# Kernel tuning notes

Hardware: AMD Instinct MI355X
Metric: run time of the kernel (lower is better)

Reference implementation:

```python
import jax, jax.numpy as jnp
import numpy as np

N_HEADS = 16
ROPE_BASE = 10000.0

def rotate_half(x):
    x1, x2 = jnp.split(x, 2, axis=-1)
    return jnp.concatenate([-x2, x1], axis=-1)

def rope_cos_sin(seq_len, head_dim, dtype):
    inv_freq = 1.0 / (ROPE_BASE ** (jnp.arange(0, head_dim, 2, dtype=jnp.float32) / head_dim))
    t = jnp.arange(seq_len, dtype=jnp.float32)
    freqs = jnp.einsum('i,j->ij', t, inv_freq)           # [S, hd/2]
    emb = jnp.concatenate([freqs, freqs], axis=-1)        # [S, hd]
    return jnp.cos(emb).astype(dtype), jnp.sin(emb).astype(dtype)

def setup_inputs() -> dict:
    key = jax.random.key(0)
    ks = jax.random.split(key, 5)
    B, S, D = 2, 2048, 2048
    x = jax.random.normal(ks[0], (B, S, D), dtype=jnp.float32)
    Wq = jax.random.normal(ks[1], (D, D), dtype=jnp.float32) * (D ** -0.5)
    Wk = jax.random.normal(ks[2], (D, D), dtype=jnp.float32) * (D ** -0.5)
    Wv = jax.random.normal(ks[3], (D, D), dtype=jnp.float32) * (D ** -0.5)
    Wo = jax.random.normal(ks[4], (D, D), dtype=jnp.float32) * (D ** -0.5)
    return {'x': x, 'Wq': Wq, 'Wk': Wk, 'Wv': Wv, 'Wo': Wo}

def reference(x, Wq, Wk, Wv, Wo):
    B, S, D = x.shape
    H = N_HEADS
    hd = D // H
    scale = hd ** -0.5
    # projections (torch Linear: x @ W.T), split heads -> [B, H, S, hd]
    def proj(W):
        return (x @ W.T).reshape(B, S, H, hd).transpose(0, 2, 1, 3)
    q, k, v = proj(Wq), proj(Wk), proj(Wv)
    # RoPE
    cos, sin = rope_cos_sin(S, hd, x.dtype)               # [S, hd]
    cos = cos[None, None, :, :]
    sin = sin[None, None, :, :]
    q = q * cos + rotate_half(q) * sin
    k = k * cos + rotate_half(k) * sin
    # scores + causal mask + fp32 softmax
    scores = jnp.einsum('bhqd,bhkd->bhqk', q, k) * scale
    causal = jnp.triu(jnp.ones((S, S), dtype=bool), k=1)  # True above diag
    scores = jnp.where(causal[None, None, :, :], -jnp.inf, scores)
    attn = jax.nn.softmax(scores.astype(jnp.float32), axis=-1).astype(q.dtype)
    out = jnp.einsum('bhqk,bhkd->bhqd', attn, v)
    out = out.transpose(0, 2, 1, 3).reshape(B, S, D)
    return out @ Wo.T
```

## Files before the change

### kernel.cpp

```cpp
#include <hip/hip_runtime.h>
#include <hip/hip_bf16.h>
#include <math.h>

#define BB 2
#define SS 2048
#define DD 2048
#define HH 16
#define HD 128
#define MM (BB * SS)
#define SCALE 0.08838834764831845f

typedef __attribute__((ext_vector_type(8))) __bf16 bf16x8;
typedef __attribute__((ext_vector_type(4))) float f32x4;
typedef __attribute__((ext_vector_type(8))) unsigned short ushort8v;

__device__ __forceinline__ float bf2f(unsigned short u) {
    union { unsigned int u; float f; } x;
    x.u = ((unsigned int)u) << 16;
    return x.f;
}
__device__ __forceinline__ unsigned short f2bf(float f) {
    union { float f; unsigned int u; } x;
    x.f = f;
    unsigned int r = x.u + 0x7FFFu + ((x.u >> 16) & 1u);
    return (unsigned short)(r >> 16);
}

__global__ __launch_bounds__(256) void cast_all(const float* __restrict__ x,
                                                const float* __restrict__ Wq,
                                                const float* __restrict__ Wk,
                                                const float* __restrict__ Wv,
                                                const float* __restrict__ Wo,
                                                unsigned short* __restrict__ xb,
                                                unsigned short* __restrict__ wqb) {
    int bid = blockIdx.x;
    const float* src;
    unsigned short* dst;
    int idx;
    if (bid < 8192) {
        src = x; dst = xb;
        idx = bid * 256 + threadIdx.x;
    } else {
        int seg = (bid - 8192) >> 12;
        idx = ((bid - 8192) & 4095) * 256 + threadIdx.x;
        src = (seg == 0) ? Wq : (seg == 1) ? Wk : (seg == 2) ? Wv : Wo;
        dst = wqb + (size_t)seg * ((size_t)DD * DD);
    }
    float4 v = ((const float4*)src)[idx];
    ushort4 o;
    o.x = f2bf(v.x); o.y = f2bf(v.y); o.z = f2bf(v.z); o.w = f2bf(v.w);
    ((ushort4*)dst)[idx] = o;
}

__global__ __launch_bounds__(64) void rope_table_kernel(float* __restrict__ cost,
                                                        float* __restrict__ sint) {
    int s = blockIdx.x;
    int i = threadIdx.x;
    float inv = powf(10000.0f, -((float)(2 * i) / 128.0f));
    float ang = (float)s * inv;
    cost[s * 64 + i] = cosf(ang);
    sint[s * 64 + i] = sinf(ang);
}

#define GEMM_BODY(A_, W_, m0_, n0_, K_, ACC_)                                      \
    for (int k0 = 0; k0 < (K_); k0 += 32) {                                        \
        __syncthreads();                                                           \
        _Pragma("unroll")                                                          \
        for (int i = 0; i < 2; ++i) {                                              \
            int c = 2 * w + i;                                                     \
            int row = c * 16 + (l >> 2);                                           \
            const unsigned short* ga = (A_) + (size_t)((m0_) + row) * (K_) + k0 + (l & 3) * 8; \
            __builtin_amdgcn_global_load_lds(                                      \
                (const __attribute__((address_space(1))) unsigned int*)ga,         \
                (__attribute__((address_space(3))) unsigned int*)(As + c * 512),   \
                16, 0, 0);                                                         \
            const unsigned short* gb = (W_) + (size_t)((n0_) + row) * (K_) + k0 + (l & 3) * 8; \
            __builtin_amdgcn_global_load_lds(                                      \
                (const __attribute__((address_space(1))) unsigned int*)gb,         \
                (__attribute__((address_space(3))) unsigned int*)(Bs + c * 512),   \
                16, 0, 0);                                                         \
        }                                                                          \
        __syncthreads();                                                           \
        bf16x8 af[4], bfr[4];                                                      \
        _Pragma("unroll")                                                          \
        for (int i = 0; i < 4; ++i) {                                              \
            af[i]  = *(const bf16x8*)&As[(wr + i * 16 + rlane) * 32 + g * 8];      \
            bfr[i] = *(const bf16x8*)&Bs[(wc + i * 16 + rlane) * 32 + g * 8];      \
        }                                                                          \
        _Pragma("unroll")                                                          \
        for (int i = 0; i < 4; ++i)                                                \
            _Pragma("unroll")                                                      \
            for (int j = 0; j < 4; ++j)                                            \
                ACC_[i][j] = __builtin_amdgcn_mfma_f32_16x16x32_bf16(af[i], bfr[j], ACC_[i][j], 0, 0, 0); \
    }

__global__ __launch_bounds__(256) void gemm_qkv(const unsigned short* __restrict__ A,
                                                const unsigned short* __restrict__ Wc,
                                                unsigned short* __restrict__ qkv) {
    __shared__ unsigned short As[128 * 32];
    __shared__ unsigned short Bs[128 * 32];
    int t = threadIdx.x, w = t >> 6, l = t & 63;
    int rlane = l & 15, g = l >> 4;
    int flat = (int)blockIdx.y * 48 + (int)blockIdx.x;
    int swz = (flat & 7) * 192 + (flat >> 3);
    int n0 = (swz % 48) * 128;
    int m0 = (swz / 48) * 128;
    int wr = (w >> 1) * 64, wc = (w & 1) * 64;
    f32x4 acc[4][4] = {};
    GEMM_BODY(A, Wc, m0, n0, 2048, acc)
    unsigned short* base = qkv + (size_t)(n0 >> 11) * ((size_t)MM * DD);
    int nc0 = n0 & 2047;
#pragma unroll
    for (int i = 0; i < 4; ++i)
#pragma unroll
        for (int r = 0; r < 4; ++r) {
            int row = m0 + wr + i * 16 + g * 4 + r;
#pragma unroll
            for (int j = 0; j < 4; ++j) {
                int col = nc0 + wc + j * 16 + rlane;
                base[(size_t)row * DD + col] = f2bf(acc[i][j][r]);
            }
        }
}

__global__ __launch_bounds__(256) void gemm_out(const unsigned short* __restrict__ A,
                                                const unsigned short* __restrict__ W,
                                                float* __restrict__ C) {
    __shared__ unsigned short As[128 * 32];
    __shared__ unsigned short Bs[128 * 32];
    int t = threadIdx.x, w = t >> 6, l = t & 63;
    int rlane = l & 15, g = l >> 4;
    int flat = (int)blockIdx.y * 16 + (int)blockIdx.x;
    int swz = (flat & 7) * 64 + (flat >> 3);
    int n0 = (swz % 16) * 128;
    int m0 = (swz / 16) * 128;
    int wr = (w >> 1) * 64, wc = (w & 1) * 64;
    f32x4 acc[4][4] = {};
    GEMM_BODY(A, W, m0, n0, 2048, acc)
#pragma unroll
    for (int i = 0; i < 4; ++i)
#pragma unroll
        for (int r = 0; r < 4; ++r) {
            int row = m0 + wr + i * 16 + g * 4 + r;
#pragma unroll
            for (int j = 0; j < 4; ++j) {
                int col = n0 + wc + j * 16 + rlane;
                C[(size_t)row * DD + col] = acc[i][j][r];
            }
        }
}

__global__ __launch_bounds__(256) void rope_apply_kernel(unsigned short* __restrict__ arr,
                                                         const float* __restrict__ cost,
                                                         const float* __restrict__ sint) {
    int idx = blockIdx.x * 256 + threadIdx.x;
    int i4 = (idx & 15) * 4;
    int h = (idx >> 4) & 15;
    int row = idx >> 8;
    int s = row & (SS - 1);
    float4 c  = *(const float4*)&cost[s * 64 + i4];
    float4 sn = *(const float4*)&sint[s * 64 + i4];
    size_t p0 = (size_t)row * DD + h * HD + i4;
    ushort4 lo = *(ushort4*)&arr[p0];
    ushort4 hi = *(ushort4*)&arr[p0 + 64];
    ushort4 olo, ohi;
    olo.x = f2bf(bf2f(lo.x) * c.x - bf2f(hi.x) * sn.x);
    olo.y = f2bf(bf2f(lo.y) * c.y - bf2f(hi.y) * sn.y);
    olo.z = f2bf(bf2f(lo.z) * c.z - bf2f(hi.z) * sn.z);
    olo.w = f2bf(bf2f(lo.w) * c.w - bf2f(hi.w) * sn.w);
    ohi.x = f2bf(bf2f(hi.x) * c.x + bf2f(lo.x) * sn.x);
    ohi.y = f2bf(bf2f(hi.y) * c.y + bf2f(lo.y) * sn.y);
    ohi.z = f2bf(bf2f(hi.z) * c.z + bf2f(lo.z) * sn.z);
    ohi.w = f2bf(bf2f(hi.w) * c.w + bf2f(lo.w) * sn.w);
    *(ushort4*)&arr[p0] = olo;
    *(ushort4*)&arr[p0 + 64] = ohi;
}

__global__ __launch_bounds__(256, 3) void mfma_attn(const unsigned short* __restrict__ qm,
                                                    const unsigned short* __restrict__ km,
                                                    const unsigned short* __restrict__ vm,
                                                    unsigned short* __restrict__ om) {
    __shared__ unsigned short Ks[2][64 * 128];
    __shared__ unsigned short Vt[128 * 64];
    __shared__ unsigned short Ps[4][16 * 40];

    int t = threadIdx.x;
    int w = t >> 6;
    int l = t & 63;
    int l15 = l & 15;
    int g = l >> 4;

    int pj = blockIdx.x;
    int h = blockIdx.y;
    int b = blockIdx.z;
    size_t bbase = (size_t)b * SS * DD + (size_t)h * HD;

    int vk0 = 2 * (t >> 3);
    int vd8 = t & 7;
    int cbase = (l15 >> 2) & 3;
    int gsw = (g ^ (l15 & 3)) * 8;

    auto stage_k = [&](int kt2, int buf) {
#pragma unroll
        for (int s = 0; s < 4; ++s) {
            int row = w * 16 + s * 4 + (l >> 4);
            int c = ((l >> 2) & 3) ^ s;
            int gg = (l & 3) ^ (l >> 4);
            const unsigned short* ga = km + bbase +
                (size_t)(kt2 * 64 + row) * DD + c * 32 + gg * 8;
            __builtin_amdgcn_global_load_lds(
                (const __attribute__((address_space(1))) unsigned int*)ga,
                (__attribute__((address_space(3))) unsigned int*)(&Ks[buf][(w * 16 + s * 4) * 128]),
                16, 0, 0);
        }
    };

    ushort8v va[2], vb[2];
    auto load_v = [&](int kt2) {
        const unsigned short* vsrc = vm + bbase + (size_t)(kt2 * 64 + vk0) * DD + vd8 * 8;
        va[0] = *(const ushort8v*)(vsrc);
        vb[0] = *(const ushort8v*)(vsrc + DD);
        va[1] = *(const ushort8v*)(vsrc + 64);
        vb[1] = *(const ushort8v*)(vsrc + DD + 64);
    };
    auto write_v = [&]() {
#pragma unroll
        for (int i = 0; i < 2; ++i)
#pragma unroll
            for (int j = 0; j < 8; ++j) {
                int d = (vd8 + 8 * i) * 8 + j;
                int swz = (vk0 >> 3) ^ ((d >> 3) & 7);
                unsigned int pack = (unsigned int)va[i][j] | ((unsigned int)vb[i][j] << 16);
                *(unsigned int*)&Vt[d * 64 + swz * 8 + (vk0 & 7)] = pack;
            }
    };

#pragma unroll 1
    for (int half = 0; half < 2; ++half) {
        int qt = half ? pj : (31 - pj);
        int q0 = qt * 64;

        bf16x8 qf[4];
        {
            int qrow = q0 + w * 16 + l15;
#pragma unroll
            for (int c = 0; c < 4; ++c)
                qf[c] = *(const bf16x8*)(qm + bbase + (size_t)qrow * DD + c * 32 + g * 8);
        }

        f32x4 acc_o[8] = {};
        float m_ = -INFINITY;
        float l_ = 0.0f;
        int nt = qt + 1;

        stage_k(0, 0);
        load_v(0);
        write_v();
        __syncthreads();

        for (int kt = 0; kt < nt; ++kt) {
            int cur = kt & 1;
            bool pref = (kt + 1 < nt);
            if (pref) {
                stage_k(kt + 1, cur ^ 1);
                load_v(kt + 1);
            }

            f32x4 s_[4] = {};
            __builtin_amdgcn_s_setprio(1);
#pragma unroll
            for (int c = 0; c < 4; ++c) {
                int coff = ((c ^ cbase) * 32) + gsw;
#pragma unroll
                for (int kg = 0; kg < 4; ++kg) {
                    bf16x8 kf = *(const bf16x8*)&Ks[cur][(kg * 16 + l15) * 128 + coff];
                    s_[kg] = __builtin_amdgcn_mfma_f32_16x16x32_bf16(kf, qf[c], s_[kg], 0, 0, 0);
                }
            }
            __builtin_amdgcn_s_setprio(0);

            float p[16];
            int qrel = w * 16 + l15;
            bool diag = (kt == qt);
#pragma unroll
            for (int kg = 0; kg < 4; ++kg)
#pragma unroll
                for (int r = 0; r < 4; ++r) {
                    float sv = s_[kg][r] * SCALE;
                    if (diag && (kg * 16 + g * 4 + r > qrel)) sv = -INFINITY;
                    p[kg * 4 + r] = sv;
                }
            float mt01 = fmaxf(fmaxf(p[0], p[1]), fmaxf(p[2], p[3]));
            float mt23 = fmaxf(fmaxf(p[4], p[5]), fmaxf(p[6], p[7]));
            float mt45 = fmaxf(fmaxf(p[8], p[9]), fmaxf(p[10], p[11]));
            float mt67 = fmaxf(fmaxf(p[12], p[13]), fmaxf(p[14], p[15]));
            float mt = fmaxf(fmaxf(mt01, mt23), fmaxf(mt45, mt67));
            mt = fmaxf(mt, __shfl_xor(mt, 16));
            mt = fmaxf(mt, __shfl_xor(mt, 32));
            if (!__all(mt - m_ <= 8.0f)) {
                float mnew = fmaxf(m_, mt);
                float alpha = __expf(m_ - mnew);
                float ar[4];
#pragma unroll
                for (int r = 0; r < 4; ++r) ar[r] = __shfl(alpha, 4 * g + r);
#pragma unroll
                for (int dg = 0; dg < 8; ++dg)
#pragma unroll
                    for (int r = 0; r < 4; ++r) acc_o[dg][r] *= ar[r];
                l_ *= alpha;
                m_ = mnew;
            }
            float ps = 0.0f;
#pragma unroll
            for (int n = 0; n < 16; ++n) {
                p[n] = __expf(p[n] - m_);
                ps += p[n];
            }
            ps += __shfl_xor(ps, 16);
            ps += __shfl_xor(ps, 32);
            l_ += ps;

            __builtin_amdgcn_s_setprio(1);
#pragma unroll
            for (int ks = 0; ks < 2; ++ks) {
#pragma unroll
                for (int kh = 0; kh < 2; ++kh) {
                    int kg = 2 * ks + kh;
                    union { __bf16 hv[4]; uint2 u2; } pk;
#pragma unroll
                    for (int r = 0; r < 4; ++r) pk.hv[r] = (__bf16)p[kg * 4 + r];
                    *(uint2*)&Ps[w][l15 * 40 + kh * 16 + g * 4] = pk.u2;
                }
                bf16x8 pf = *(const bf16x8*)&Ps[w][l15 * 40 + g * 8];
#pragma unroll
                for (int dg = 0; dg < 8; ++dg) {
                    int d = dg * 16 + l15;
                    int swz = (ks * 4 + g) ^ ((d >> 3) & 7);
                    bf16x8 vf = *(const bf16x8*)&Vt[d * 64 + swz * 8];
                    acc_o[dg] = __builtin_amdgcn_mfma_f32_16x16x32_bf16(pf, vf, acc_o[dg], 0, 0, 0);
                }
            }
            __builtin_amdgcn_s_setprio(0);

            __syncthreads();
            if (pref) write_v();
            __syncthreads();
        }

        float lr[4];
#pragma unroll
        for (int r = 0; r < 4; ++r) lr[r] = 1.0f / __shfl(l_, 4 * g + r);
#pragma unroll
        for (int dg = 0; dg < 8; ++dg)
#pragma unroll
            for (int r = 0; r < 4; ++r) {
                int qrow2 = q0 + w * 16 + g * 4 + r;
                om[bbase + (size_t)qrow2 * DD + dg * 16 + l15] =
                    f2bf(acc_o[dg][r] * lr[r]);
            }
    }
}

extern "C" void kernel_launch(void* const* d_in, const int* in_sizes, int n_in,
                              void* d_out, int out_size, void* d_ws, size_t ws_size,
                              hipStream_t stream) {
    const float* x  = (const float*)d_in[0];
    const float* Wq = (const float*)d_in[1];
    const float* Wk = (const float*)d_in[2];
    const float* Wv = (const float*)d_in[3];
    const float* Wo = (const float*)d_in[4];
    float* out = (float*)d_out;

    char* ws = (char*)d_ws;
    const size_t MD = (size_t)MM * DD;
    const size_t WN = (size_t)DD * DD;
    unsigned short* qb   = (unsigned short*)(ws);
    unsigned short* kb   = (unsigned short*)(ws + 2 * MD);
    unsigned short* vb   = (unsigned short*)(ws + 4 * MD);
    unsigned short* ctxb = (unsigned short*)(ws + 6 * MD);
    unsigned short* xb   = (unsigned short*)(ws + 8 * MD);
    unsigned short* wqb  = (unsigned short*)(ws + 10 * MD);
    unsigned short* wob  = (unsigned short*)(ws + 10 * MD + 6 * WN);
    float* cost = (float*)(ws + 10 * MD + 8 * WN);
    float* sint = cost + SS * 64;

    cast_all<<<8192 + 4 * 4096, 256, 0, stream>>>(x, Wq, Wk, Wv, Wo, xb, wqb);

    rope_table_kernel<<<SS, 64, 0, stream>>>(cost, sint);

    gemm_qkv<<<dim3(48, 32), 256, 0, stream>>>(xb, wqb, qb);

    rope_apply_kernel<<<2 * MM * HH * 16 / 256, 256, 0, stream>>>(qb, cost, sint);

    mfma_attn<<<dim3(16, HH, BB), 256, 0, stream>>>(qb, kb, vb, ctxb);

    gemm_out<<<dim3(16, 32), 256, 0, stream>>>(ctxb, wob, out);
}
```

Before: 402.9 us.

## Double query rows per warp in attention to reuse K/V tiles across two MFMA groups

Each attention block now processes a 128-row query tile, with each warp owning two 16-row query groups. Each K and V fragment read from LDS therefore feeds two MFMAs, halving LDS traffic and K/V staging per query row. The grid is flattened and assigns query tiles reversed for one batch to spread causal work, replacing the previous paired-tile scheme. The costs are higher register use (launch bounds lowered to 2 blocks per CU), a larger P scratch buffer in LDS, and a changed swizzle for the transposed V tile.

```diff
diff --git a/kernel.cpp b/kernel.cpp
--- a/kernel.cpp
+++ b/kernel.cpp
@@ -176,13 +176,13 @@
     *(ushort4*)&arr[p0 + 64] = ohi;
 }
 
-__global__ __launch_bounds__(256, 3) void mfma_attn(const unsigned short* __restrict__ qm,
+__global__ __launch_bounds__(256, 2) void mfma_attn(const unsigned short* __restrict__ qm,
                                                     const unsigned short* __restrict__ km,
                                                     const unsigned short* __restrict__ vm,
                                                     unsigned short* __restrict__ om) {
     __shared__ unsigned short Ks[2][64 * 128];
     __shared__ unsigned short Vt[128 * 64];
-    __shared__ unsigned short Ps[4][16 * 40];
+    __shared__ unsigned short Ps[4][32 * 72];
 
     int t = threadIdx.x;
     int w = t >> 6;
@@ -190,9 +190,12 @@
     int l15 = l & 15;
     int g = l >> 4;
 
-    int pj = blockIdx.x;
-    int h = blockIdx.y;
-    int b = blockIdx.z;
+    int gid = blockIdx.x;
+    int b = gid >> 8;
+    int h = (gid >> 4) & 15;
+    int m = gid & 15;
+    int qt = b ? m : (15 - m);
+    int q0 = qt * 128;
     size_t bbase = (size_t)b * SS * DD + (size_t)h * HD;
 
     int vk0 = 2 * (t >> 3);
@@ -229,134 +232,144 @@
 #pragma unroll
             for (int j = 0; j < 8; ++j) {
                 int d = (vd8 + 8 * i) * 8 + j;
-                int swz = (vk0 >> 3) ^ ((d >> 3) & 7);
+                int slot = j ^ vd8 ^ (vk0 >> 3);
                 unsigned int pack = (unsigned int)va[i][j] | ((unsigned int)vb[i][j] << 16);
-                *(unsigned int*)&Vt[d * 64 + swz * 8 + (vk0 & 7)] = pack;
+                *(unsigned int*)&Vt[d * 64 + slot * 8 + (vk0 & 7)] = pack;
             }
     };
 
-#pragma unroll 1
-    for (int half = 0; half < 2; ++half) {
-        int qt = half ? pj : (31 - pj);
-        int q0 = qt * 64;
-
-        bf16x8 qf[4];
-        {
-            int qrow = q0 + w * 16 + l15;
-#pragma unroll
-            for (int c = 0; c < 4; ++c)
-                qf[c] = *(const bf16x8*)(qm + bbase + (size_t)qrow * DD + c * 32 + g * 8);
-        }
-
-        f32x4 acc_o[8] = {};
-        float m_ = -INFINITY;
-        float l_ = 0.0f;
-        int nt = qt + 1;
-
-        stage_k(0, 0);
-        load_v(0);
-        write_v();
-        __syncthreads();
-
-        for (int kt = 0; kt < nt; ++kt) {
-            int cur = kt & 1;
-            bool pref = (kt + 1 < nt);
-            if (pref) {
-                stage_k(kt + 1, cur ^ 1);
-                load_v(kt + 1);
-            }
-
-            f32x4 s_[4] = {};
-            __builtin_amdgcn_s_setprio(1);
-#pragma unroll
-            for (int c = 0; c < 4; ++c) {
-                int coff = ((c ^ cbase) * 32) + gsw;
-#pragma unroll
-                for (int kg = 0; kg < 4; ++kg) {
-                    bf16x8 kf = *(const bf16x8*)&Ks[cur][(kg * 16 + l15) * 128 + coff];
-                    s_[kg] = __builtin_amdgcn_mfma_f32_16x16x32_bf16(kf, qf[c], s_[kg], 0, 0, 0);
+    bf16x8 qf[2][4];
+#pragma unroll
+    for (int qg = 0; qg < 2; ++qg) {
+        int qrow = q0 + w * 32 + qg * 16 + l15;
+#pragma unroll
+        for (int c = 0; c < 4; ++c)
+            qf[qg][c] = *(const bf16x8*)(qm + bbase + (size_t)qrow * DD + c * 32 + g * 8);
+    }
+
+    f32x4 acc_o[2][8] = {};
+    float m_[2] = {-INFINITY, -INFINITY};
+    float l_[2] = {0.0f, 0.0f};
+    int nt = 2 * qt + 2;
+
+    stage_k(0, 0);
+    load_v(0);
+    write_v();
+    __syncthreads();
+
+    for (int kt = 0; kt < nt; ++kt) {
+        int cur = kt & 1;
+        bool pref = (kt + 1 < nt);
+        if (pref) {
+            stage_k(kt + 1, cur ^ 1);
+            load_v(kt + 1);
+        }
+
+        f32x4 s_[2][4] = {};
+        __builtin_amdgcn_s_setprio(1);
+#pragma unroll
+        for (int c = 0; c < 4; ++c) {
+            int coff = ((c ^ cbase) * 32) + gsw;
+#pragma unroll
+            for (int kg = 0; kg < 4; ++kg) {
+                bf16x8 kf = *(const bf16x8*)&Ks[cur][(kg * 16 + l15) * 128 + coff];
+#pragma unroll
+                for (int qg = 0; qg < 2; ++qg)
+                    s_[qg][kg] = __builtin_amdgcn_mfma_f32_16x16x32_bf16(
+                        kf, qf[qg][c], s_[qg][kg], 0, 0, 0);
+            }
+        }
+        __builtin_amdgcn_s_setprio(0);
+
+        float p[2][16];
+        bool maskt = (kt >= 2 * qt);
+#pragma unroll
+        for (int qg = 0; qg < 2; ++qg) {
+            int qglob = q0 + w * 32 + qg * 16 + l15;
+#pragma unroll
+            for (int kg = 0; kg < 4; ++kg)
+#pragma unroll
+                for (int r = 0; r < 4; ++r) {
+                    float sv = s_[qg][kg][r] * SCALE;
+                    if (maskt && (kt * 64 + kg * 16 + g * 4 + r > qglob)) sv = -INFINITY;
+                    p[qg][kg * 4 + r] = sv;
                 }
-            }
-            __builtin_amdgcn_s_setprio(0);
-
-            float p[16];
-            int qrel = w * 16 + l15;
-            bool diag = (kt == qt);
-#pragma unroll
-            for (int kg = 0; kg < 4; ++kg)
-#pragma unroll
-                for (int r = 0; r < 4; ++r) {
-                    float sv = s_[kg][r] * SCALE;
-                    if (diag && (kg * 16 + g * 4 + r > qrel)) sv = -INFINITY;
-                    p[kg * 4 + r] = sv;
-                }
-            float mt01 = fmaxf(fmaxf(p[0], p[1]), fmaxf(p[2], p[3]));
-            float mt23 = fmaxf(fmaxf(p[4], p[5]), fmaxf(p[6], p[7]));
-            float mt45 = fmaxf(fmaxf(p[8], p[9]), fmaxf(p[10], p[11]));
-            float mt67 = fmaxf(fmaxf(p[12], p[13]), fmaxf(p[14], p[15]));
+            float mt01 = fmaxf(fmaxf(p[qg][0], p[qg][1]), fmaxf(p[qg][2], p[qg][3]));
+            float mt23 = fmaxf(fmaxf(p[qg][4], p[qg][5]), fmaxf(p[qg][6], p[qg][7]));
+            float mt45 = fmaxf(fmaxf(p[qg][8], p[qg][9]), fmaxf(p[qg][10], p[qg][11]));
+            float mt67 = fmaxf(fmaxf(p[qg][12], p[qg][13]), fmaxf(p[qg][14], p[qg][15]));
             float mt = fmaxf(fmaxf(mt01, mt23), fmaxf(mt45, mt67));
             mt = fmaxf(mt, __shfl_xor(mt, 16));
             mt = fmaxf(mt, __shfl_xor(mt, 32));
-            if (!__all(mt - m_ <= 8.0f)) {
-                float mnew = fmaxf(m_, mt);
-                float alpha = __expf(m_ - mnew);
+            if (!__all(mt - m_[qg] <= 8.0f)) {
+                float mnew = fmaxf(m_[qg], mt);
+                float alpha = __expf(m_[qg] - mnew);
                 float ar[4];
 #pragma unroll
                 for (int r = 0; r < 4; ++r) ar[r] = __shfl(alpha, 4 * g + r);
 #pragma unroll
                 for (int dg = 0; dg < 8; ++dg)
 #pragma unroll
-                    for (int r = 0; r < 4; ++r) acc_o[dg][r] *= ar[r];
-                l_ *= alpha;
-                m_ = mnew;
+                    for (int r = 0; r < 4; ++r) acc_o[qg][dg][r] *= ar[r];
+                l_[qg] *= alpha;
+                m_[qg] = mnew;
             }
             float ps = 0.0f;
 #pragma unroll
             for (int n = 0; n < 16; ++n) {
-                p[n] = __expf(p[n] - m_);
-                ps += p[n];
+                p[qg][n] = __expf(p[qg][n] - m_[qg]);
+                ps += p[qg][n];
             }
             ps += __shfl_xor(ps, 16);
             ps += __shfl_xor(ps, 32);
-            l_ += ps;
-
-            __builtin_amdgcn_s_setprio(1);
-#pragma unroll
-            for (int ks = 0; ks < 2; ++ks) {
-#pragma unroll
-                for (int kh = 0; kh < 2; ++kh) {
-                    int kg = 2 * ks + kh;
-                    union { __bf16 hv[4]; uint2 u2; } pk;
-#pragma unroll
-                    for (int r = 0; r < 4; ++r) pk.hv[r] = (__bf16)p[kg * 4 + r];
-                    *(uint2*)&Ps[w][l15 * 40 + kh * 16 + g * 4] = pk.u2;
-                }
-                bf16x8 pf = *(const bf16x8*)&Ps[w][l15 * 40 + g * 8];
-#pragma unroll
-                for (int dg = 0; dg < 8; ++dg) {
-                    int d = dg * 16 + l15;
-                    int swz = (ks * 4 + g) ^ ((d >> 3) & 7);
-                    bf16x8 vf = *(const bf16x8*)&Vt[d * 64 + swz * 8];
-                    acc_o[dg] = __builtin_amdgcn_mfma_f32_16x16x32_bf16(pf, vf, acc_o[dg], 0, 0, 0);
-                }
-            }
-            __builtin_amdgcn_s_setprio(0);
-
-            __syncthreads();
-            if (pref) write_v();
-            __syncthreads();
-        }
-
+            l_[qg] += ps;
+
+#pragma unroll
+            for (int kg = 0; kg < 4; ++kg) {
+                union { __bf16 hv[4]; uint2 u2; } pk;
+#pragma unroll
+                for (int r = 0; r < 4; ++r) pk.hv[r] = (__bf16)p[qg][kg * 4 + r];
+                *(uint2*)&Ps[w][(qg * 16 + l15) * 72 + kg * 16 + g * 4] = pk.u2;
+            }
+        }
+
+        __builtin_amdgcn_s_setprio(1);
+#pragma unroll
+        for (int ks = 0; ks < 2; ++ks) {
+            bf16x8 pf[2];
+#pragma unroll
+            for (int qg = 0; qg < 2; ++qg)
+                pf[qg] = *(const bf16x8*)&Ps[w][(qg * 16 + l15) * 72 + ks * 32 + g * 8];
+#pragma unroll
+            for (int dg = 0; dg < 8; ++dg) {
+                int d = dg * 16 + l15;
+                int slot = (l15 & 7) ^ ((2 * dg + (l15 >> 3)) & 7) ^ (ks * 4 + g);
+                bf16x8 vf = *(const bf16x8*)&Vt[d * 64 + slot * 8];
+#pragma unroll
+                for (int qg = 0; qg < 2; ++qg)
+                    acc_o[qg][dg] = __builtin_amdgcn_mfma_f32_16x16x32_bf16(
+                        pf[qg], vf, acc_o[qg][dg], 0, 0, 0);
+            }
+        }
+        __builtin_amdgcn_s_setprio(0);
+
+        __syncthreads();
+        if (pref) write_v();
+        __syncthreads();
+    }
+
+#pragma unroll
+    for (int qg = 0; qg < 2; ++qg) {
         float lr[4];
 #pragma unroll
-        for (int r = 0; r < 4; ++r) lr[r] = 1.0f / __shfl(l_, 4 * g + r);
+        for (int r = 0; r < 4; ++r) lr[r] = 1.0f / __shfl(l_[qg], 4 * g + r);
 #pragma unroll
         for (int dg = 0; dg < 8; ++dg)
 #pragma unroll
             for (int r = 0; r < 4; ++r) {
-                int qrow2 = q0 + w * 16 + g * 4 + r;
+                int qrow2 = q0 + w * 32 + qg * 16 + g * 4 + r;
                 om[bbase + (size_t)qrow2 * DD + dg * 16 + l15] =
-                    f2bf(acc_o[dg][r] * lr[r]);
+                    f2bf(acc_o[qg][dg][r] * lr[r]);
             }
     }
 }
@@ -392,7 +405,7 @@
 
     rope_apply_kernel<<<2 * MM * HH * 16 / 256, 256, 0, stream>>>(qb, cost, sint);
 
-    mfma_attn<<<dim3(16, HH, BB), 256, 0, stream>>>(qb, kb, vb, ctxb);
+    mfma_attn<<<512, 256, 0, stream>>>(qb, kb, vb, ctxb);
 
     gemm_out<<<dim3(16, 32), 256, 0, stream>>>(ctxb, wob, out);
 }
```

New measurement: 412.6 us. +2.4%, slower.
